# Performance work log

Measured on AMD Instinct MI355X. Metric: run time of the kernel, lower is better.

Reference implementation:

```python
import jax, jax.numpy as jnp
import numpy as np

B, T, S, E, H = 2, 2048, 2048, 1024, 16
DH = E // H

def setup_inputs() -> dict:
    key = jax.random.key(0)
    ks = jax.random.split(key, 12)
    sc = 1.0 / np.sqrt(E)
    inp = {
        'query': jax.random.normal(ks[0], (B, T, E), jnp.float32),
        'key':   jax.random.normal(ks[1], (B, S, E), jnp.float32),
        'value': jax.random.normal(ks[2], (B, S, E), jnp.float32),
        'Wq': jax.random.normal(ks[3], (E, E), jnp.float32) * sc,
        'bq': jnp.zeros((E,), jnp.float32),
        'Wk': jax.random.normal(ks[4], (E, E), jnp.float32) * sc,
        'bk': jnp.zeros((E,), jnp.float32),
        'Wv': jax.random.normal(ks[5], (E, E), jnp.float32) * sc,
        'bv': jnp.zeros((E,), jnp.float32),
        'Wo': jax.random.normal(ks[6], (E, E), jnp.float32) * sc,
        'bo': jnp.zeros((E,), jnp.float32),
    }
    return inp

def reference(query, key, value, Wq, bq, Wk, bk, Wv, bv, Wo, bo):
    # Linear projections (torch nn.Linear: x @ W.T + b)
    Q = query @ Wq.T + bq          # [B,T,E]
    K = key   @ Wk.T + bk          # [B,S,E]
    V = value @ Wv.T + bv          # [B,S,E]
    # split heads -> [B,H,L,DH]
    Q = Q.reshape(B, T, H, DH).transpose(0, 2, 1, 3)
    K = K.reshape(B, S, H, DH).transpose(0, 2, 1, 3)
    V = V.reshape(B, S, H, DH).transpose(0, 2, 1, 3)
    scores = jnp.einsum('bhtd,bhsd->bhts', Q, K) / jnp.sqrt(jnp.float32(DH))
    attn = jax.nn.softmax(scores, axis=-1)            # [B,H,T,S]
    out = jnp.einsum('bhts,bhsd->bhtd', attn, V)      # [B,H,T,DH]
    out = out.transpose(0, 2, 1, 3).reshape(B, T, E)
    out = out @ Wo.T + bo                             # [B,T,E]
    attn_avg = attn.mean(axis=1)                      # average_attn_weights=True
    return out, attn_avg
```

## Files before the change

kernel.cpp:

```cpp
#include <hip/hip_runtime.h>

#define DEV __device__ __forceinline__

typedef __attribute__((ext_vector_type(8))) short short8;
typedef __attribute__((ext_vector_type(4))) float floatx4;
typedef __attribute__((ext_vector_type(2))) unsigned int uint2v;
typedef unsigned short u16;

DEV u16 f2bf(float f) {
  unsigned int u = __float_as_uint(f);
  u += 0x7fffu + ((u >> 16) & 1u);
  return (u16)(u >> 16);
}

DEV unsigned int cvtpk(float a, float b) {
  unsigned int r;
  asm("v_cvt_pk_bf16_f32 %0, %1, %2" : "=v"(r) : "v"(a), "v"(b));
  return r;
}

DEV void load16_to_lds(const void* g, void* l) {
  __builtin_amdgcn_global_load_lds(
      (const __attribute__((address_space(1))) unsigned int*)g,
      (__attribute__((address_space(3))) unsigned int*)l, 16, 0, 0);
}

DEV int xcd_swz(int flat, int nwg) {
  return (flat & 7) * (nwg >> 3) + (flat >> 3);
}

#define MFMA16(A, B, C) __builtin_amdgcn_mfma_f32_16x16x32_bf16(A, B, C, 0, 0, 0)
#define EXP2(x) __builtin_amdgcn_exp2f(x)

#define QSCALE 0.18033688011112042f

DEV void stage_block(const u16* src_row0, int k0, int ln, void* ldsbase) {
  int r = ln >> 2;
  int p = ((ln & 3) - (ln >> 4)) & 3;
  load16_to_lds((const char*)(src_row0 + (size_t)r * 1024 + k0) + p * 16, ldsbase);
}
DEV const short8* frag_addr(const u16* base, int blk, int c, int q) {
  int slot = c * 4 + ((q + (c >> 2)) & 3);
  return (const short8*)(base + blk * 512 + slot * 8);
}

__global__ __launch_bounds__(256) void cvt_all(
    const float* __restrict__ w0, const float* __restrict__ w1,
    const float* __restrict__ w2, const float* __restrict__ w3,
    const float* __restrict__ a0, const float* __restrict__ a1, const float* __restrict__ a2,
    u16* __restrict__ e0, u16* __restrict__ e1, u16* __restrict__ e2, u16* __restrict__ e3,
    u16* __restrict__ f0, u16* __restrict__ f1, u16* __restrict__ f2) {
  const int t = blockIdx.y;
  const float* s;
  u16* d;
  size_t base;
  if (t < 4) {
    s = t == 0 ? w0 : t == 1 ? w1 : t == 2 ? w2 : w3;
    d = t == 0 ? e0 : t == 1 ? e1 : t == 2 ? e2 : e3;
    base = 0;
  } else {
    int a = (t - 4) >> 2;
    s = a == 0 ? a0 : a == 1 ? a1 : a2;
    d = a == 0 ? f0 : a == 1 ? f1 : f2;
    base = (size_t)((t - 4) & 3) * 1048576;
  }
  size_t i = base + (size_t)(blockIdx.x * 256 + threadIdx.x) * 4;
  float4 v = *(const float4*)(s + i);
  ushort4 o;
  o.x = f2bf(v.x); o.y = f2bf(v.y); o.z = f2bf(v.z); o.w = f2bf(v.w);
  *(ushort4*)(d + i) = o;
}

__global__ __launch_bounds__(256) void qkv_gemm(
    const u16* __restrict__ qb, const u16* __restrict__ kb, const u16* __restrict__ vb,
    const u16* __restrict__ wq, const u16* __restrict__ wk, const u16* __restrict__ wv,
    const float* __restrict__ bq, const float* __restrict__ bk, const float* __restrict__ bv,
    u16* __restrict__ Qh, u16* __restrict__ Kh, u16* __restrict__ VT) {
  __shared__ __align__(16) u16 As[2][4096];
  __shared__ __align__(16) u16 Bs[2][4096];
  const int tid = threadIdx.x;
  const int w = tid >> 6, ln = tid & 63, q = ln >> 4, c = ln & 15;
  const int wr = w >> 1, wc = w & 1;
  const int lg = xcd_swz(blockIdx.x + 8 * blockIdx.y + 256 * blockIdx.z, 768);
  const int lbx = lg & 7, lby = (lg >> 3) & 31, z = lg >> 8;
  const int m0 = (z == 2 ? lbx : lby) * 128;
  const int n0 = (z == 2 ? lby : lbx) * 128;
  const u16* Asrc = z == 0 ? qb : (z == 1 ? kb : wv);
  const u16* Bsrc = z == 0 ? wq : (z == 1 ? wk : vb);

  floatx4 acc[4][4];
#pragma unroll
  for (int i = 0; i < 4; ++i)
#pragma unroll
    for (int j = 0; j < 4; ++j) acc[i][j] = (floatx4){0.f, 0.f, 0.f, 0.f};

#pragma unroll
  for (int it = 0; it < 2; ++it) {
    int I = w * 2 + it;
    stage_block(Asrc + (size_t)(m0 + I * 16) * 1024, 0, ln, (char*)As[0] + I * 1024);
    stage_block(Bsrc + (size_t)(n0 + I * 16) * 1024, 0, ln, (char*)Bs[0] + I * 1024);
  }

  int cur = 0;
  for (int k0 = 0; k0 < 1024; k0 += 32) {
    __syncthreads();
    if (k0 + 32 < 1024) {
      const int nb = cur ^ 1;
#pragma unroll
      for (int it = 0; it < 2; ++it) {
        int I = w * 2 + it;
        stage_block(Asrc + (size_t)(m0 + I * 16) * 1024, k0 + 32, ln, (char*)As[nb] + I * 1024);
        stage_block(Bsrc + (size_t)(n0 + I * 16) * 1024, k0 + 32, ln, (char*)Bs[nb] + I * 1024);
      }
    }
    short8 a[4], bb[4];
#pragma unroll
    for (int mt = 0; mt < 4; ++mt) a[mt] = *frag_addr(As[cur], wr * 4 + mt, c, q);
#pragma unroll
    for (int nt = 0; nt < 4; ++nt) bb[nt] = *frag_addr(Bs[cur], wc * 4 + nt, c, q);
    __builtin_amdgcn_s_setprio(1);
#pragma unroll
    for (int mt = 0; mt < 4; ++mt)
#pragma unroll
      for (int nt = 0; nt < 4; ++nt) acc[mt][nt] = MFMA16(a[mt], bb[nt], acc[mt][nt]);
    __builtin_amdgcn_s_setprio(0);
    cur ^= 1;
  }

  if (z <= 1) {
    const float* bias = z ? bk : bq;
    u16* dst = z ? Kh : Qh;
    const float scale = z ? 1.0f : QSCALE;
    float bn[4];
#pragma unroll
    for (int nt = 0; nt < 4; ++nt) bn[nt] = bias[n0 + wc * 64 + nt * 16 + c];
#pragma unroll
    for (int mt = 0; mt < 4; ++mt)
#pragma unroll
      for (int r = 0; r < 4; ++r) {
        int m = m0 + wr * 64 + mt * 16 + 4 * q + r;
        int bbv = m >> 11, t = m & 2047;
#pragma unroll
        for (int nt = 0; nt < 4; ++nt) {
          int n = n0 + wc * 64 + nt * 16 + c;
          dst[((size_t)(bbv * 16 + (n >> 6)) * 2048 + t) * 64 + (n & 63)] =
              f2bf((acc[mt][nt][r] + bn[nt]) * scale);
        }
      }
  } else {
    float bm[4][4];
#pragma unroll
    for (int mt = 0; mt < 4; ++mt)
#pragma unroll
      for (int r = 0; r < 4; ++r) bm[mt][r] = bv[m0 + wr * 64 + mt * 16 + 4 * q + r];
#pragma unroll
    for (int mt = 0; mt < 4; ++mt)
#pragma unroll
      for (int r = 0; r < 4; ++r) {
        int d = m0 + wr * 64 + mt * 16 + 4 * q + r;
        int hh = d >> 6, dl = d & 63;
#pragma unroll
        for (int nt = 0; nt < 4; ++nt) {
          int s = n0 + wc * 64 + nt * 16 + c;
          int bbv = s >> 11, sl = s & 2047;
          VT[((size_t)(bbv * 16 + hh) * 64 + dl) * 2048 + sl] = f2bf(acc[mt][nt][r] + bm[mt][r]);
        }
      }
  }
}

__global__ __launch_bounds__(256) void oproj_gemm(const u16* __restrict__ Ap, const u16* __restrict__ Wp,
                                                  const float* __restrict__ bias, float* __restrict__ out) {
  __shared__ __align__(16) u16 As[2][4096];
  __shared__ __align__(16) u16 Bs[2][2048];
  const int tid = threadIdx.x;
  const int w = tid >> 6, ln = tid & 63, q = ln >> 4, c = ln & 15;
  const int wr = w >> 1, wc = w & 1;
  const int lg = xcd_swz(blockIdx.x + 16 * blockIdx.y, 512);
  const int n0 = (lg & 15) * 64, m0 = (lg >> 4) * 128;

  floatx4 acc[4][2];
#pragma unroll
  for (int i = 0; i < 4; ++i)
#pragma unroll
    for (int j = 0; j < 2; ++j) acc[i][j] = (floatx4){0.f, 0.f, 0.f, 0.f};

#pragma unroll
  for (int j = 0; j < 3; ++j) {
    int idx = w * 3 + j;
    if (idx < 8) {
      stage_block(Ap + (size_t)(m0 + idx * 16) * 1024, 0, ln, (char*)As[0] + idx * 1024);
    } else {
      int bi = idx - 8;
      stage_block(Wp + (size_t)(n0 + bi * 16) * 1024, 0, ln, (char*)Bs[0] + bi * 1024);
    }
  }

  int cur = 0;
  for (int k0 = 0; k0 < 1024; k0 += 32) {
    __syncthreads();
    if (k0 + 32 < 1024) {
      const int nb = cur ^ 1;
#pragma unroll
      for (int j = 0; j < 3; ++j) {
        int idx = w * 3 + j;
        if (idx < 8) {
          stage_block(Ap + (size_t)(m0 + idx * 16) * 1024, k0 + 32, ln, (char*)As[nb] + idx * 1024);
        } else {
          int bi = idx - 8;
          stage_block(Wp + (size_t)(n0 + bi * 16) * 1024, k0 + 32, ln, (char*)Bs[nb] + bi * 1024);
        }
      }
    }
    short8 a[4], bb[2];
#pragma unroll
    for (int mt = 0; mt < 4; ++mt) a[mt] = *frag_addr(As[cur], wr * 4 + mt, c, q);
#pragma unroll
    for (int nt = 0; nt < 2; ++nt) bb[nt] = *frag_addr(Bs[cur], wc * 2 + nt, c, q);
    __builtin_amdgcn_s_setprio(1);
#pragma unroll
    for (int mt = 0; mt < 4; ++mt)
#pragma unroll
      for (int nt = 0; nt < 2; ++nt) acc[mt][nt] = MFMA16(a[mt], bb[nt], acc[mt][nt]);
    __builtin_amdgcn_s_setprio(0);
    cur ^= 1;
  }

  float bn[2];
#pragma unroll
  for (int nt = 0; nt < 2; ++nt) bn[nt] = bias[n0 + wc * 32 + nt * 16 + c];
#pragma unroll
  for (int mt = 0; mt < 4; ++mt)
#pragma unroll
    for (int r = 0; r < 4; ++r) {
      int m = m0 + wr * 64 + mt * 16 + 4 * q + r;
#pragma unroll
      for (int nt = 0; nt < 2; ++nt)
        out[(size_t)m * 1024 + n0 + wc * 32 + nt * 16 + c] = acc[mt][nt][r] + bn[nt];
    }
}

__global__ __launch_bounds__(512, 4) void flash_attn(const u16* __restrict__ Qh, const u16* __restrict__ Kh,
                                                     const u16* __restrict__ VhT, u16* __restrict__ Obuf,
                                                     float* __restrict__ l_ws) {
  __shared__ __align__(16) u16 Ks[2][4096];
  __shared__ __align__(16) u16 VTs[2][4096];
  __shared__ __align__(16) u16 Ps[8][1152];
  const int tid = threadIdx.x;
  const int w = tid >> 6, ln = tid & 63, q = ln >> 4, c = ln & 15;
  const int lg = xcd_swz(blockIdx.x + 16 * (blockIdx.y + 16 * blockIdx.z), 512);
  const int t0 = (lg & 15) * 128, h = (lg >> 4) & 15, b = lg >> 8;
  const size_t bh = (size_t)(b * 16 + h);
  const u16* Qbase = Qh + bh * 131072;
  const u16* Kbase = Kh + bh * 131072;
  const u16* Vbase = VhT + bh * 131072;

  short8 qf0, qf1;
  {
    const u16* qr = Qbase + (size_t)(t0 + w * 16 + c) * 64 + q * 8;
    qf0 = *(const short8*)qr;
    qf1 = *(const short8*)(qr + 32);
  }
  floatx4 oacc[4];
  float lacc = 0.f;
#pragma unroll
  for (int j = 0; j < 4; ++j) oacc[j] = (floatx4){0.f, 0.f, 0.f, 0.f};

  const int srow = ln >> 3;
  const int sch = (ln & 7) ^ srow;
  const int cx = c & 7;
  const int row = w * 8 + srow;

  load16_to_lds((const char*)Kbase + ((size_t)row * 64 + sch * 8) * 2, (char*)Ks[0] + w * 1024);
  load16_to_lds((const char*)Vbase + ((size_t)row * 2048 + sch * 8) * 2, (char*)VTs[0] + w * 1024);

  int cur = 0;
  for (int s0 = 0; s0 < 2048; s0 += 64) {
    __syncthreads();
    if (s0 + 64 < 2048) {
      const int nb = cur ^ 1;
      load16_to_lds((const char*)Kbase + ((size_t)(s0 + 64 + row) * 64 + sch * 8) * 2,
                    (char*)Ks[nb] + w * 1024);
      load16_to_lds((const char*)Vbase + ((size_t)row * 2048 + (s0 + 64) + sch * 8) * 2,
                    (char*)VTs[nb] + w * 1024);
    }
    const u16* ks = Ks[cur];
    const u16* vs = VTs[cur];
#pragma unroll
    for (int st = 0; st < 4; ++st) {
      const int rr = st * 16 + c;
      short8 k0 = *(const short8*)(ks + rr * 64 + ((q ^ cx) << 3));
      short8 k1 = *(const short8*)(ks + rr * 64 + (((4 + q) ^ cx) << 3));
      floatx4 zz = (floatx4){0.f, 0.f, 0.f, 0.f};
      __builtin_amdgcn_s_setprio(1);
      zz = MFMA16(k0, qf0, zz);
      zz = MFMA16(k1, qf1, zz);
      __builtin_amdgcn_s_setprio(0);
      float e0 = EXP2(zz[0]), e1 = EXP2(zz[1]), e2 = EXP2(zz[2]), e3 = EXP2(zz[3]);
      lacc += (e0 + e1) + (e2 + e3);
      uint2v pk = {cvtpk(e0, e1), cvtpk(e2, e3)};
      *(uint2v*)(&Ps[w][c * 72 + st * 16 + 4 * q]) = pk;
    }
    short8 pf0 = *(const short8*)(&Ps[w][c * 72 + q * 8]);
    short8 pf1 = *(const short8*)(&Ps[w][c * 72 + 32 + q * 8]);
    __builtin_amdgcn_s_setprio(1);
#pragma unroll
    for (int dt = 0; dt < 4; ++dt) {
      const int rr = dt * 16 + c;
      short8 v0 = *(const short8*)(vs + rr * 64 + ((q ^ cx) << 3));
      short8 v1 = *(const short8*)(vs + rr * 64 + (((4 + q) ^ cx) << 3));
      oacc[dt] = MFMA16(pf0, v0, oacc[dt]);
      oacc[dt] = MFMA16(pf1, v1, oacc[dt]);
    }
    __builtin_amdgcn_s_setprio(0);
    cur ^= 1;
  }
  {
    float v = lacc;
    v += __shfl_xor(v, 16);
    v += __shfl_xor(v, 32);
    lacc = v;
    if (q == 0) l_ws[bh * 2048 + t0 + w * 16 + c] = v;
  }
#pragma unroll
  for (int r = 0; r < 4; ++r) {
    float lv = __shfl(lacc, 4 * q + r);
    float inv = __builtin_amdgcn_rcpf(lv);
    const int t = t0 + w * 16 + 4 * q + r;
#pragma unroll
    for (int dt = 0; dt < 4; ++dt)
      Obuf[((size_t)b * 2048 + t) * 1024 + h * 64 + dt * 16 + c] = f2bf(oacc[dt][r] * inv);
  }
}

__global__ __launch_bounds__(256) void attn_avg_k(const u16* __restrict__ Qh, const u16* __restrict__ Kh,
                                                  const float* __restrict__ l_ws, float* __restrict__ out2) {
  __shared__ __align__(16) u16 Ks[2][4096];
  const int tid = threadIdx.x;
  const int w = tid >> 6, ln = tid & 63, q = ln >> 4, c = ln & 15;
  const int lg = xcd_swz(blockIdx.x + 32 * (blockIdx.y + 16 * blockIdx.z), 1024);
  const int s0 = (lg & 31) * 64, t0 = ((lg >> 5) & 15) * 128, b = lg >> 9;
  const int srow = ln >> 3;
  const int sch = (ln & 7) ^ srow;
  const int cx = c & 7;

  floatx4 acc[2][4];
#pragma unroll
  for (int i = 0; i < 2; ++i)
#pragma unroll
    for (int j = 0; j < 4; ++j) acc[i][j] = (floatx4){0.f, 0.f, 0.f, 0.f};

#pragma unroll
  for (int it = 0; it < 2; ++it) {
    int I = w * 2 + it;
    int row = I * 8 + srow;
    load16_to_lds((const char*)(Kh + (size_t)(b * 16) * 131072) + ((size_t)(s0 + row) * 64 + sch * 8) * 2,
                  (char*)Ks[0] + I * 1024);
  }

  for (int h = 0; h < 16; ++h) {
    const size_t bh = (size_t)(b * 16 + h);
    const u16* ks = Ks[h & 1];
    __syncthreads();
    if (h < 15) {
      const u16* Kn = Kh + (bh + 1) * 131072;
#pragma unroll
      for (int it = 0; it < 2; ++it) {
        int I = w * 2 + it;
        int row = I * 8 + srow;
        load16_to_lds((const char*)Kn + ((size_t)(s0 + row) * 64 + sch * 8) * 2,
                      (char*)Ks[(h + 1) & 1] + I * 1024);
      }
    }
    short8 qf[2][2];
    float linv[2];
#pragma unroll
    for (int blk = 0; blk < 2; ++blk) {
      const u16* qr = Qh + bh * 131072 + (size_t)(t0 + w * 32 + blk * 16 + c) * 64 + q * 8;
      qf[blk][0] = *(const short8*)qr;
      qf[blk][1] = *(const short8*)(qr + 32);
      linv[blk] = __builtin_amdgcn_rcpf(l_ws[bh * 2048 + t0 + w * 32 + blk * 16 + c]) * 0.0625f;
    }
#pragma unroll
    for (int st = 0; st < 4; ++st) {
      const int row = st * 16 + c;
      short8 k0 = *(const short8*)(ks + row * 64 + ((q ^ cx) << 3));
      short8 k1 = *(const short8*)(ks + row * 64 + (((4 + q) ^ cx) << 3));
#pragma unroll
      for (int blk = 0; blk < 2; ++blk) {
        floatx4 zz = (floatx4){0.f, 0.f, 0.f, 0.f};
        zz = MFMA16(k0, qf[blk][0], zz);
        zz = MFMA16(k1, qf[blk][1], zz);
#pragma unroll
        for (int r = 0; r < 4; ++r) acc[blk][st][r] += EXP2(zz[r]) * linv[blk];
      }
    }
  }
#pragma unroll
  for (int blk = 0; blk < 2; ++blk) {
    const size_t t = (size_t)t0 + w * 32 + blk * 16 + c;
#pragma unroll
    for (int st = 0; st < 4; ++st) {
      float4 o;
      o.x = acc[blk][st][0]; o.y = acc[blk][st][1]; o.z = acc[blk][st][2]; o.w = acc[blk][st][3];
      *(float4*)(out2 + ((size_t)b * 2048 + t) * 2048 + s0 + st * 16 + 4 * q) = o;
    }
  }
}

extern "C" void kernel_launch(void* const* d_in, const int* in_sizes, int n_in,
                              void* d_out, int out_size, void* d_ws, size_t ws_size,
                              hipStream_t stream) {
  const float* query = (const float*)d_in[0];
  const float* key = (const float*)d_in[1];
  const float* value = (const float*)d_in[2];
  const float* Wq = (const float*)d_in[3];
  const float* bq = (const float*)d_in[4];
  const float* Wk = (const float*)d_in[5];
  const float* bk = (const float*)d_in[6];
  const float* Wv = (const float*)d_in[7];
  const float* bv = (const float*)d_in[8];
  const float* Wo = (const float*)d_in[9];
  const float* bo = (const float*)d_in[10];

  char* ws = (char*)d_ws;
  const size_t MB = 1024 * 1024;
  u16* wWq = (u16*)(ws + 0 * MB);
  u16* wWk = (u16*)(ws + 2 * MB);
  u16* wWv = (u16*)(ws + 4 * MB);
  u16* wWo = (u16*)(ws + 6 * MB);
  u16* wQh = (u16*)(ws + 8 * MB);
  u16* wKh = (u16*)(ws + 16 * MB);
  u16* wVT = (u16*)(ws + 24 * MB);
  u16* wO = (u16*)(ws + 32 * MB);
  float* wl = (float*)(ws + 40 * MB);
  float* out = (float*)d_out;
  float* out2 = out + (size_t)4194304;

  u16* qb = (u16*)out2;
  u16* kb = qb + 4194304;
  u16* vb = kb + 4194304;

  cvt_all<<<dim3(1024, 16), 256, 0, stream>>>(Wq, Wk, Wv, Wo, query, key, value,
                                              wWq, wWk, wWv, wWo, qb, kb, vb);
  qkv_gemm<<<dim3(8, 32, 3), 256, 0, stream>>>(qb, kb, vb, wWq, wWk, wWv,
                                               bq, bk, bv, wQh, wKh, wVT);
  flash_attn<<<dim3(16, 16, 2), 512, 0, stream>>>(wQh, wKh, wVT, wO, wl);
  attn_avg_k<<<dim3(32, 16, 2), 256, 0, stream>>>(wQh, wKh, wl, out2);
  oproj_gemm<<<dim3(16, 32), 256, 0, stream>>>(wO, wWo, bo, out);
}
```

Baseline: 276.6 us.

## Enlarge QKV and output projection GEMM tiles to 256x128 with 512-thread blocks

Both projection GEMMs now use 512-thread blocks with 8 waves, each computing a 256x128 output tile. Previously the QKV GEMM used 128x128 tiles and the output projection 128x64 tiles. Larger tiles raise arithmetic intensity and cut redundant global loads. The XCD swizzle is removed, and the grid shrinks to half or a quarter as many blocks, which may lower occupancy and L2 locality. The change also touches the epilogue index mapping, so the hidden epilogue code must stay consistent with the new wr range of 0..3.

```diff
diff --git a/kernel.cpp b/kernel.cpp
--- a/kernel.cpp
+++ b/kernel.cpp
@@ -71,20 +71,27 @@
   *(ushort4*)(d + i) = o;
 }
 
-__global__ __launch_bounds__(256) void qkv_gemm(
+__global__ __launch_bounds__(512, 4) void qkv_gemm(
     const u16* __restrict__ qb, const u16* __restrict__ kb, const u16* __restrict__ vb,
     const u16* __restrict__ wq, const u16* __restrict__ wk, const u16* __restrict__ wv,
     const float* __restrict__ bq, const float* __restrict__ bk, const float* __restrict__ bv,
     u16* __restrict__ Qh, u16* __restrict__ Kh, u16* __restrict__ VT) {
-  __shared__ __align__(16) u16 As[2][4096];
+  __shared__ __align__(16) u16 As[2][8192];
   __shared__ __align__(16) u16 Bs[2][4096];
   const int tid = threadIdx.x;
   const int w = tid >> 6, ln = tid & 63, q = ln >> 4, c = ln & 15;
   const int wr = w >> 1, wc = w & 1;
-  const int lg = xcd_swz(blockIdx.x + 8 * blockIdx.y + 256 * blockIdx.z, 768);
-  const int lbx = lg & 7, lby = (lg >> 3) & 31, z = lg >> 8;
-  const int m0 = (z == 2 ? lbx : lby) * 128;
-  const int n0 = (z == 2 ? lby : lbx) * 128;
+  const int z = blockIdx.z;
+  int m_idx, n_idx;
+  if (z == 2) {
+    int f2 = blockIdx.x + 8 * blockIdx.y;
+    n_idx = f2 & 31;
+    m_idx = f2 >> 5;
+  } else {
+    n_idx = blockIdx.x;
+    m_idx = blockIdx.y;
+  }
+  const int m0 = m_idx * 256, n0 = n_idx * 128;
   const u16* Asrc = z == 0 ? qb : (z == 1 ? kb : wv);
   const u16* Bsrc = z == 0 ? wq : (z == 1 ? wk : vb);
 
@@ -95,10 +102,12 @@
     for (int j = 0; j < 4; ++j) acc[i][j] = (floatx4){0.f, 0.f, 0.f, 0.f};
 
 #pragma unroll
-  for (int it = 0; it < 2; ++it) {
-    int I = w * 2 + it;
-    stage_block(Asrc + (size_t)(m0 + I * 16) * 1024, 0, ln, (char*)As[0] + I * 1024);
-    stage_block(Bsrc + (size_t)(n0 + I * 16) * 1024, 0, ln, (char*)Bs[0] + I * 1024);
+  for (int j = 0; j < 3; ++j) {
+    int idx = w * 3 + j;
+    if (idx < 16)
+      stage_block(Asrc + (size_t)(m0 + idx * 16) * 1024, 0, ln, (char*)As[0] + idx * 1024);
+    else
+      stage_block(Bsrc + (size_t)(n0 + (idx - 16) * 16) * 1024, 0, ln, (char*)Bs[0] + (idx - 16) * 1024);
   }
 
   int cur = 0;
@@ -107,10 +116,13 @@
     if (k0 + 32 < 1024) {
       const int nb = cur ^ 1;
 #pragma unroll
-      for (int it = 0; it < 2; ++it) {
-        int I = w * 2 + it;
-        stage_block(Asrc + (size_t)(m0 + I * 16) * 1024, k0 + 32, ln, (char*)As[nb] + I * 1024);
-        stage_block(Bsrc + (size_t)(n0 + I * 16) * 1024, k0 + 32, ln, (char*)Bs[nb] + I * 1024);
+      for (int j = 0; j < 3; ++j) {
+        int idx = w * 3 + j;
+        if (idx < 16)
+          stage_block(Asrc + (size_t)(m0 + idx * 16) * 1024, k0 + 32, ln, (char*)As[nb] + idx * 1024);
+        else
+          stage_block(Bsrc + (size_t)(n0 + (idx - 16) * 16) * 1024, k0 + 32, ln,
+                      (char*)Bs[nb] + (idx - 16) * 1024);
       }
     }
     short8 a[4], bb[4];
@@ -169,31 +181,28 @@
   }
 }
 
-__global__ __launch_bounds__(256) void oproj_gemm(const u16* __restrict__ Ap, const u16* __restrict__ Wp,
-                                                  const float* __restrict__ bias, float* __restrict__ out) {
-  __shared__ __align__(16) u16 As[2][4096];
-  __shared__ __align__(16) u16 Bs[2][2048];
+__global__ __launch_bounds__(512, 4) void oproj_gemm(const u16* __restrict__ Ap, const u16* __restrict__ Wp,
+                                                     const float* __restrict__ bias, float* __restrict__ out) {
+  __shared__ __align__(16) u16 As[2][8192];
+  __shared__ __align__(16) u16 Bs[2][4096];
   const int tid = threadIdx.x;
   const int w = tid >> 6, ln = tid & 63, q = ln >> 4, c = ln & 15;
   const int wr = w >> 1, wc = w & 1;
-  const int lg = xcd_swz(blockIdx.x + 16 * blockIdx.y, 512);
-  const int n0 = (lg & 15) * 64, m0 = (lg >> 4) * 128;
-
-  floatx4 acc[4][2];
+  const int n0 = blockIdx.x * 128, m0 = blockIdx.y * 256;
+
+  floatx4 acc[4][4];
 #pragma unroll
   for (int i = 0; i < 4; ++i)
 #pragma unroll
-    for (int j = 0; j < 2; ++j) acc[i][j] = (floatx4){0.f, 0.f, 0.f, 0.f};
+    for (int j = 0; j < 4; ++j) acc[i][j] = (floatx4){0.f, 0.f, 0.f, 0.f};
 
 #pragma unroll
   for (int j = 0; j < 3; ++j) {
     int idx = w * 3 + j;
-    if (idx < 8) {
+    if (idx < 16)
       stage_block(Ap + (size_t)(m0 + idx * 16) * 1024, 0, ln, (char*)As[0] + idx * 1024);
-    } else {
-      int bi = idx - 8;
-      stage_block(Wp + (size_t)(n0 + bi * 16) * 1024, 0, ln, (char*)Bs[0] + bi * 1024);
-    }
+    else
+      stage_block(Wp + (size_t)(n0 + (idx - 16) * 16) * 1024, 0, ln, (char*)Bs[0] + (idx - 16) * 1024);
   }
 
   int cur = 0;
@@ -204,39 +213,38 @@
 #pragma unroll
       for (int j = 0; j < 3; ++j) {
         int idx = w * 3 + j;
-        if (idx < 8) {
+        if (idx < 16)
           stage_block(Ap + (size_t)(m0 + idx * 16) * 1024, k0 + 32, ln, (char*)As[nb] + idx * 1024);
-        } else {
-          int bi = idx - 8;
-          stage_block(Wp + (size_t)(n0 + bi * 16) * 1024, k0 + 32, ln, (char*)Bs[nb] + bi * 1024);
-        }
-      }
-    }
-    short8 a[4], bb[2];
+        else
+          stage_block(Wp + (size_t)(n0 + (idx - 16) * 16) * 1024, k0 + 32, ln,
+                      (char*)Bs[nb] + (idx - 16) * 1024);
+      }
+    }
+    short8 a[4], bb[4];
 #pragma unroll
     for (int mt = 0; mt < 4; ++mt) a[mt] = *frag_addr(As[cur], wr * 4 + mt, c, q);
 #pragma unroll
-    for (int nt = 0; nt < 2; ++nt) bb[nt] = *frag_addr(Bs[cur], wc * 2 + nt, c, q);
+    for (int nt = 0; nt < 4; ++nt) bb[nt] = *frag_addr(Bs[cur], wc * 4 + nt, c, q);
     __builtin_amdgcn_s_setprio(1);
 #pragma unroll
     for (int mt = 0; mt < 4; ++mt)
 #pragma unroll
-      for (int nt = 0; nt < 2; ++nt) acc[mt][nt] = MFMA16(a[mt], bb[nt], acc[mt][nt]);
+      for (int nt = 0; nt < 4; ++nt) acc[mt][nt] = MFMA16(a[mt], bb[nt], acc[mt][nt]);
     __builtin_amdgcn_s_setprio(0);
     cur ^= 1;
   }
 
-  float bn[2];
-#pragma unroll
-  for (int nt = 0; nt < 2; ++nt) bn[nt] = bias[n0 + wc * 32 + nt * 16 + c];
+  float bn[4];
+#pragma unroll
+  for (int nt = 0; nt < 4; ++nt) bn[nt] = bias[n0 + wc * 64 + nt * 16 + c];
 #pragma unroll
   for (int mt = 0; mt < 4; ++mt)
 #pragma unroll
     for (int r = 0; r < 4; ++r) {
       int m = m0 + wr * 64 + mt * 16 + 4 * q + r;
 #pragma unroll
-      for (int nt = 0; nt < 2; ++nt)
-        out[(size_t)m * 1024 + n0 + wc * 32 + nt * 16 + c] = acc[mt][nt][r] + bn[nt];
+      for (int nt = 0; nt < 4; ++nt)
+        out[(size_t)m * 1024 + n0 + wc * 64 + nt * 16 + c] = acc[mt][nt][r] + bn[nt];
     }
 }
 
@@ -443,9 +451,9 @@
 
   cvt_all<<<dim3(1024, 16), 256, 0, stream>>>(Wq, Wk, Wv, Wo, query, key, value,
                                               wWq, wWk, wWv, wWo, qb, kb, vb);
-  qkv_gemm<<<dim3(8, 32, 3), 256, 0, stream>>>(qb, kb, vb, wWq, wWk, wWv,
+  qkv_gemm<<<dim3(8, 16, 3), 512, 0, stream>>>(qb, kb, vb, wWq, wWk, wWv,
                                                bq, bk, bv, wQh, wKh, wVT);
   flash_attn<<<dim3(16, 16, 2), 512, 0, stream>>>(wQh, wKh, wVT, wO, wl);
   attn_avg_k<<<dim3(32, 16, 2), 256, 0, stream>>>(wQh, wKh, wl, out2);
-  oproj_gemm<<<dim3(16, 32), 256, 0, stream>>>(wO, wWo, bo, out);
-}
+  oproj_gemm<<<dim3(8, 16), 512, 0, stream>>>(wO, wWo, bo, out);
+}
```

Result: no change. 280.3 us (+1.3%).
